# Kernel tuning notes

Measured on AMD Instinct MI355X. Metric: run time of the kernel, lower is better.

## Reference

```python
import jax, jax.numpy as jnp
import numpy as np

N_NODES = 100000


def gcn_conv(x, W, b, src, dst, n):
    # PyG GCNConv: linear transform, add self-loops, symmetric deg^-1/2 norm,
    # scatter-sum messages from src -> dst, add bias.
    x = x @ W  # [N, out]
    loop = jnp.arange(n, dtype=src.dtype)
    src_sl = jnp.concatenate([src, loop])
    dst_sl = jnp.concatenate([dst, loop])
    deg = jax.ops.segment_sum(jnp.ones_like(dst_sl, dtype=x.dtype), dst_sl, num_segments=n)
    dinv = jax.lax.rsqrt(deg)
    norm = dinv[src_sl] * dinv[dst_sl]  # [E+N]
    msg = x[src_sl] * norm[:, None]
    out = jax.ops.segment_sum(msg, dst_sl, num_segments=n)
    return out + b


def base_gnn(x, edge_index, W1, b1, W2, b2):
    src, dst = edge_index[0], edge_index[1]
    n = x.shape[0]
    h = gcn_conv(x, W1, b1, src, dst, n)
    h = jax.nn.relu(h)
    return gcn_conv(h, W2, b2, src, dst, n)


def setup_inputs() -> dict:
    key = jax.random.key(0)
    ks = jax.random.split(key, 12)
    n, e, ep, en = N_NODES, 1600000, 200000, 200000
    in_ch, hid, out_ch, n_classes = 256, 128, 128, 10
    x = jax.random.normal(ks[0], (n, in_ch), dtype=jnp.float32)
    edge_index = jax.random.randint(ks[1], (2, e), 0, n, dtype=jnp.int64)
    edge_index_pos = jax.random.randint(ks[2], (2, ep), 0, n, dtype=jnp.int64)
    edge_index_neg = jax.random.randint(ks[3], (2, en), 0, n, dtype=jnp.int64)
    s1 = 1.0 / np.sqrt(in_ch)
    s2 = 1.0 / np.sqrt(hid)
    so = 1.0 / np.sqrt(out_ch)
    sl = 1.0 / np.sqrt(2 * out_ch)
    return {
        "x": x,
        "edge_index": edge_index,
        "edge_index_pos": edge_index_pos,
        "edge_index_neg": edge_index_neg,
        "W1": jax.random.uniform(ks[4], (in_ch, hid), jnp.float32, -s1, s1),
        "b1": jnp.zeros((hid,), jnp.float32),
        "W2": jax.random.uniform(ks[5], (hid, out_ch), jnp.float32, -s2, s2),
        "b2": jnp.zeros((out_ch,), jnp.float32),
        "Wcls": jax.random.uniform(ks[6], (out_ch, n_classes), jnp.float32, -so, so),
        "bcls": jax.random.uniform(ks[7], (n_classes,), jnp.float32, -so, so),
        "Wlink": jax.random.uniform(ks[8], (2 * out_ch, 1), jnp.float32, -sl, sl),
        "blink": jax.random.uniform(ks[9], (1,), jnp.float32, -sl, sl),
    }


def reference(x, edge_index, edge_index_pos, edge_index_neg,
              W1, b1, W2, b2, Wcls, bcls, Wlink, blink):
    # Shared base embedding (math identical to torch's redundant recompute)
    h = base_gnn(x, edge_index, W1, b1, W2, b2)  # [N, 128]
    # Node head
    node_logits = jax.nn.relu(h) @ Wcls + bcls
    node_pred = jax.nn.log_softmax(node_logits, axis=1)
    # Link head: gather endpoint embeddings, concat, linear
    xp = jnp.concatenate([h[edge_index_pos[0]], h[edge_index_pos[1]]], axis=1)
    xn = jnp.concatenate([h[edge_index_neg[0]], h[edge_index_neg[1]]], axis=1)
    link_pos = (xp @ Wlink + blink)[:, 0]
    link_neg = (xn @ Wlink + blink)[:, 0]
    return (node_pred, link_pos, link_neg)
```

## Files before the change

### kernel.cpp

```cpp
#include <hip/hip_runtime.h>
#include <stdint.h>

typedef __attribute__((ext_vector_type(8))) short bf16x8;
typedef __attribute__((ext_vector_type(4))) float f32x4;

__device__ __forceinline__ float b2f(uint32_t h) {
    union { uint32_t u; float f; } v; v.u = h << 16; return v.f;
}
__device__ __forceinline__ ushort f2b(float f) {
    union { float f; uint32_t u; } v; v.f = f;
    uint32_t u = v.u;
    return (ushort)((u + 0x7fffu + ((u >> 16) & 1u)) >> 16);
}
__device__ __forceinline__ float ldin(const void* p, int i, int fp32) {
    return fp32 ? ((const float*)p)[i] : b2f(((const ushort*)p)[i]);
}

__global__ void k_flags(const void* W1, const void* ei, int* flags) {
    int l = threadIdx.x;
    const ushort* w = (const ushort*)W1;
    float a0 = fabsf(b2f(w[l]));
    float a1 = fabsf(b2f(w[64 + l]));
    bool bad = !(a0 <= 0.25f) || !(a1 <= 0.25f);
    unsigned long long mb = __ballot(bad);
    const int* e = (const int*)ei;
    bool z = (l < 16) ? (e[2 * l + 1] == 0) : false;
    unsigned long long mz = __ballot(z);
    if (l == 0) {
        flags[0] = mb ? 1 : 0;
        flags[1] = (__popcll(mz & 0xffffull) >= 15) ? 1 : 0;
    }
}

__global__ __launch_bounds__(256) void k_cvt_idx(const void* ei, const void* ep, const void* en,
                                                 int* cEi, int* cEp, int* cEn,
                                                 int twoE, int twoEp, int twoEn, int N,
                                                 const int* __restrict__ flags) {
    int i = blockIdx.x * 256 + threadIdx.x;
    int i64 = flags[1];
    const void* srcp; int* dstp; int j = i;
    if (i < twoE) { srcp = ei; dstp = cEi; }
    else if (i < twoE + twoEp) { srcp = ep; dstp = cEp; j = i - twoE; }
    else if (i < twoE + twoEp + twoEn) { srcp = en; dstp = cEn; j = i - twoE - twoEp; }
    else return;
    int v = i64 ? (int)((const long long*)srcp)[j] : ((const int*)srcp)[j];
    v = v < 0 ? 0 : (v >= N ? N - 1 : v);
    dstp[j] = v;
}

__global__ __launch_bounds__(256) void k_cvt_w(const void* W1, const void* W2, const void* Wc,
                                               const void* b1, const void* b2, const void* bc,
                                               const void* Wl, const void* bl,
                                               ushort* Wt1, ushort* Wt2, ushort* WtC,
                                               ushort* b1c, ushort* b2c, ushort* bcc,
                                               ushort* Wlc, ushort* blc,
                                               const int* __restrict__ flags) {
    int i = blockIdx.x * 256 + threadIdx.x;
    int f = flags[0];
    if (i < 32768) {
        int c = i >> 8, k = i & 255;
        Wt1[i] = f2b(ldin(W1, k * 128 + c, f));
    } else if (i < 49152) {
        int j = i - 32768, c = j >> 7, k = j & 127;
        Wt2[j] = f2b(ldin(W2, k * 128 + c, f));
    } else if (i < 51200) {
        int j = i - 49152, c = j >> 7, k = j & 127;
        ushort v = 0;
        if (c < 10) v = f2b(ldin(Wc, k * 10 + c, f));
        WtC[j] = v;
    } else if (i < 51328) {
        int j = i - 51200; b1c[j] = f2b(ldin(b1, j, f));
    } else if (i < 51456) {
        int j = i - 51328; b2c[j] = f2b(ldin(b2, j, f));
    } else if (i < 51472) {
        int j = i - 51456;
        ushort v = 0;
        if (j < 10) v = f2b(ldin(bc, j, f));
        bcc[j] = v;
    } else if (i < 51728) {
        int j = i - 51472; Wlc[j] = f2b(ldin(Wl, j, f));
    } else if (i < 51736) {
        int j = i - 51728;
        ushort v = 0;
        if (j < 1) v = f2b(ldin(bl, 0, f));
        blc[j] = v;
    }
}

__global__ __launch_bounds__(256) void k_cvt_x(const void* __restrict__ x, ushort* __restrict__ xc,
                                               int N, const int* __restrict__ flags) {
    int gw = blockIdx.x * 4 + (threadIdx.x >> 6);
    int ntile = (N + 15) >> 4;
    if (gw >= ntile * 8) return;
    int tile = gw >> 3, s = gw & 7;
    int l = threadIdx.x & 63, mr = l & 15, q = l >> 4;
    int row = tile * 16 + mr;
    if (row > N - 1) row = N - 1;
    uint4 o;
    if (flags[0]) {
        const float* xf = (const float*)x + (size_t)row * 256 + s * 32 + q * 8;
        float4 a = *(const float4*)xf;
        float4 b = *(const float4*)(xf + 4);
        o.x = (uint32_t)f2b(a.x) | ((uint32_t)f2b(a.y) << 16);
        o.y = (uint32_t)f2b(a.z) | ((uint32_t)f2b(a.w) << 16);
        o.z = (uint32_t)f2b(b.x) | ((uint32_t)f2b(b.y) << 16);
        o.w = (uint32_t)f2b(b.z) | ((uint32_t)f2b(b.w) << 16);
    } else {
        o = *(const uint4*)((const ushort*)x + (size_t)row * 256 + s * 32 + q * 8);
    }
    *(uint4*)(xc + ((size_t)gw * 64 + l) * 8) = o;
}

__global__ __launch_bounds__(256) void k_hist1(const int* __restrict__ dst, int* __restrict__ histM,
                                               int E, int NB1) {
    __shared__ int h[512];
    for (int j = threadIdx.x; j < 512; j += 256) h[j] = 0;
    __syncthreads();
    int base = blockIdx.x * 4096;
    for (int j = threadIdx.x; j < 4096; j += 256) {
        int i = base + j;
        if (i < E) atomicAdd(&h[dst[i] >> 8], 1);
    }
    __syncthreads();
    for (int j = threadIdx.x; j < 512; j += 256)
        histM[j * NB1 + blockIdx.x] = h[j];
}

__global__ __launch_bounds__(1024) void k_mscan_block(const int* __restrict__ in, int* __restrict__ out,
                                                      int* __restrict__ bsum, int len) {
    __shared__ int sh[1024];
    int t = threadIdx.x;
    int i = blockIdx.x * 1024 + t;
    int val = (i < len) ? in[i] : 0;
    sh[t] = val; __syncthreads();
    for (int off = 1; off < 1024; off <<= 1) {
        int v = (t >= off) ? sh[t - off] : 0;
        __syncthreads();
        sh[t] += v;
        __syncthreads();
    }
    if (i < len) out[i] = sh[t] - val;
    if (t == 1023) bsum[blockIdx.x] = sh[1023];
}

__global__ __launch_bounds__(1024) void k_mscan_top(int* __restrict__ bsum, int nb) {
    __shared__ int sh[1024];
    int t = threadIdx.x;
    int val = (t < nb) ? bsum[t] : 0;
    sh[t] = val; __syncthreads();
    for (int off = 1; off < 1024; off <<= 1) {
        int v = (t >= off) ? sh[t - off] : 0;
        __syncthreads();
        sh[t] += v;
        __syncthreads();
    }
    if (t < nb) bsum[t] = sh[t] - val;
}

__global__ __launch_bounds__(1024) void k_mscan_add(int* __restrict__ out, const int* __restrict__ bsum, int len) {
    int i = blockIdx.x * 1024 + threadIdx.x;
    if (i < len) out[i] += bsum[blockIdx.x];
}

__global__ __launch_bounds__(512) void k_cbs(const int* __restrict__ off, int* __restrict__ cbs, int E, int NB1) {
    int t = threadIdx.x;
    cbs[t] = off[t * NB1];
    if (t == 0) cbs[512] = E;
}

__global__ __launch_bounds__(256) void k_scatter1(const int* __restrict__ src, const int* __restrict__ dst,
                                                  const int* __restrict__ off, int2* __restrict__ grouped,
                                                  int E, int NB1) {
    __shared__ int o[512];
    for (int j = threadIdx.x; j < 512; j += 256) o[j] = off[j * NB1 + blockIdx.x];
    __syncthreads();
    int base = blockIdx.x * 4096;
    for (int j = threadIdx.x; j < 4096; j += 256) {
        int i = base + j;
        if (i < E) {
            int d = dst[i];
            int p = atomicAdd(&o[d >> 8], 1);
            grouped[p] = make_int2(src[i], d);
        }
    }
}

__global__ __launch_bounds__(256) void k_deg2(const int2* __restrict__ grouped, const int* __restrict__ cbs,
                                              int* __restrict__ deg, int N) {
    __shared__ int c[256];
    c[threadIdx.x] = 0;
    __syncthreads();
    int b = blockIdx.x;
    int s0 = cbs[b], s1 = cbs[b + 1];
    for (int i = s0 + threadIdx.x; i < s1; i += 256)
        atomicAdd(&c[grouped[i].y & 255], 1);
    __syncthreads();
    int v = b * 256 + threadIdx.x;
    if (v < N) deg[v] = c[threadIdx.x];
}

__global__ __launch_bounds__(1024) void k_scan_block(const int* __restrict__ deg, int* __restrict__ rowptr,
                                                     float* __restrict__ dinv, int* __restrict__ bsum, int n) {
    __shared__ int sh[1024];
    int t = threadIdx.x;
    int i = blockIdx.x * 1024 + t;
    int val = (i < n) ? deg[i] : 0;
    sh[t] = val; __syncthreads();
    for (int off = 1; off < 1024; off <<= 1) {
        int v = (t >= off) ? sh[t - off] : 0;
        __syncthreads();
        sh[t] += v;
        __syncthreads();
    }
    if (i < n) {
        rowptr[i] = sh[t] - val;
        dinv[i] = rsqrtf((float)(val + 1));
    }
    if (t == 1023) bsum[blockIdx.x] = sh[1023];
}

__global__ __launch_bounds__(128) void k_scan_top(const int* __restrict__ bsum, int* __restrict__ boff, int nb) {
    __shared__ int sh[128];
    int t = threadIdx.x;
    int val = (t < nb) ? bsum[t] : 0;
    sh[t] = val; __syncthreads();
    for (int off = 1; off < 128; off <<= 1) {
        int v = (t >= off) ? sh[t - off] : 0;
        __syncthreads();
        sh[t] += v;
        __syncthreads();
    }
    if (t < nb) boff[t] = sh[t] - val;
}

__global__ __launch_bounds__(1024) void k_scan_add(int* __restrict__ rowptr, const int* __restrict__ boff,
                                                   int n, int E) {
    int i = blockIdx.x * 1024 + threadIdx.x;
    if (i < n) rowptr[i] += boff[blockIdx.x];
    if (i == 0) rowptr[n] = E;
}

__global__ __launch_bounds__(256) void k_fill2(const int2* __restrict__ grouped, const int* __restrict__ cbs,
                                               const int* __restrict__ rowptr, const float* __restrict__ dinv,
                                               int2* __restrict__ edge, int N) {
    __shared__ int o[256];
    int b = blockIdx.x;
    int v = b * 256 + threadIdx.x;
    o[threadIdx.x] = (v < N) ? rowptr[v] : 0;
    __syncthreads();
    int s0 = cbs[b], s1 = cbs[b + 1];
    for (int i = s0 + threadIdx.x; i < s1; i += 256) {
        int2 e = grouped[i];
        int p = atomicAdd(&o[e.y & 255], 1);
        float w = dinv[e.x] * dinv[e.y];
        edge[p] = make_int2(e.x, __float_as_int(w));
    }
}

template <int NS>
__global__ __launch_bounds__(256, 2) void k_gemm(const ushort* __restrict__ Xf,
                                                 const ushort* __restrict__ Wt,
                                                 ushort* __restrict__ Out, int nrows) {
    __shared__ uint4 sB[NS * 8 * 64];

    const int tid = threadIdx.x;
    for (int it = tid; it < NS * 8 * 64; it += 256) {
        int l = it & 63, fn = it >> 6;
        int s = fn >> 3, n = fn & 7;
        int mr = l & 15, q = l >> 4;
        sB[it] = *(const uint4*)(Wt + (size_t)(n * 16 + mr) * (NS * 32) + s * 32 + q * 8);
    }
    __syncthreads();

    const int wave = tid >> 6;
    const int l = tid & 63;
    const int q = l >> 4, mr = l & 15;
    const int gw = blockIdx.x * 4 + wave;
    const int nw = gridDim.x * 4;
    const int ntile = (nrows + 15) >> 4;

    for (int tp = gw; tp * 2 < ntile; tp += nw) {
        const int t0 = tp * 2;
        const bool has1 = (t0 + 1 < ntile);
        const int t1 = has1 ? t0 + 1 : t0;

        bf16x8 a0[NS], a1[NS];
        const ushort* x0 = Xf + ((size_t)t0 * NS * 64 + l) * 8;
        const ushort* x1 = Xf + ((size_t)t1 * NS * 64 + l) * 8;
#pragma unroll
        for (int s = 0; s < NS; ++s) a0[s] = *(const bf16x8*)(x0 + s * 512);
#pragma unroll
        for (int s = 0; s < NS; ++s) a1[s] = *(const bf16x8*)(x1 + s * 512);

        f32x4 acc0[8], acc1[8];
#pragma unroll
        for (int n = 0; n < 8; ++n) {
            acc0[n] = (f32x4){0.f, 0.f, 0.f, 0.f};
            acc1[n] = (f32x4){0.f, 0.f, 0.f, 0.f};
        }
#pragma unroll
        for (int s = 0; s < NS; ++s) {
#pragma unroll
            for (int n = 0; n < 8; ++n) {
                bf16x8 b = __builtin_bit_cast(bf16x8, sB[(s * 8 + n) * 64 + l]);
                acc0[n] = __builtin_amdgcn_mfma_f32_16x16x32_bf16(b, a0[s], acc0[n], 0, 0, 0);
                acc1[n] = __builtin_amdgcn_mfma_f32_16x16x32_bf16(b, a1[s], acc1[n], 0, 0, 0);
            }
        }
        int row0 = t0 * 16 + mr;
        if (row0 < nrows) {
            ushort* orow = Out + (size_t)row0 * 128 + q * 4;
#pragma unroll
            for (int n = 0; n < 8; ++n) {
                uint2 o;
                o.x = (uint32_t)f2b(acc0[n][0]) | ((uint32_t)f2b(acc0[n][1]) << 16);
                o.y = (uint32_t)f2b(acc0[n][2]) | ((uint32_t)f2b(acc0[n][3]) << 16);
                *(uint2*)(orow + n * 16) = o;
            }
        }
        if (has1) {
            int row1 = t1 * 16 + mr;
            if (row1 < nrows) {
                ushort* orow = Out + (size_t)row1 * 128 + q * 4;
#pragma unroll
                for (int n = 0; n < 8; ++n) {
                    uint2 o;
                    o.x = (uint32_t)f2b(acc1[n][0]) | ((uint32_t)f2b(acc1[n][1]) << 16);
                    o.y = (uint32_t)f2b(acc1[n][2]) | ((uint32_t)f2b(acc1[n][3]) << 16);
                    *(uint2*)(orow + n * 16) = o;
                }
            }
        }
    }
}

__device__ __forceinline__ void fma8(float* acc, uint4 p, float w) {
    uint32_t pu[4] = {p.x, p.y, p.z, p.w};
#pragma unroll
    for (int k = 0; k < 4; ++k) {
        float lo = __uint_as_float(pu[k] << 16);
        float hi = __uint_as_float(pu[k] & 0xffff0000u);
        acc[2 * k]     += lo * w;
        acc[2 * k + 1] += hi * w;
    }
}

__global__ __launch_bounds__(256) void k_conv(const ushort* __restrict__ XW, const int* __restrict__ rowptr,
                                              const int2* __restrict__ edge, const float* __restrict__ dinv,
                                              const ushort* __restrict__ bias, ushort* __restrict__ Hout,
                                              int n, int relu, int frag) {
    int wave = threadIdx.x >> 6;
    int v = blockIdx.x * 4 + wave;
    if (v >= n) return;
    int l = threadIdx.x & 63;
    int g = l >> 4;
    int c = l & 15;

    int s0 = rowptr[v], s1 = rowptr[v + 1];
    float dv = dinv[v];
    float wself = (g == 0) ? dv * dv : 0.f;

    uint4 pv = *(const uint4*)(XW + (size_t)v * 128 + c * 8);
    float acc[8];
    {
        uint32_t pu[4] = {pv.x, pv.y, pv.z, pv.w};
#pragma unroll
        for (int k = 0; k < 4; ++k) {
            acc[2 * k]     = __uint_as_float(pu[k] << 16) * wself;
            acc[2 * k + 1] = __uint_as_float(pu[k] & 0xffff0000u) * wself;
        }
    }

    int i = s0;
    while (i + 8 <= s1) {
        int2 eA = edge[i + g];
        int2 eB = edge[i + 4 + g];
        uint4 pA = *(const uint4*)(XW + (size_t)eA.x * 128 + c * 8);
        uint4 pB = *(const uint4*)(XW + (size_t)eB.x * 128 + c * 8);
        fma8(acc, pA, __int_as_float(eA.y));
        fma8(acc, pB, __int_as_float(eB.y));
        i += 8;
    }
    if (i + 4 <= s1) {
        int2 e = edge[i + g];
        uint4 p = *(const uint4*)(XW + (size_t)e.x * 128 + c * 8);
        fma8(acc, p, __int_as_float(e.y));
        i += 4;
    }
    if (i < s1) {
        int ei = i + g;
        bool val = ei < s1;
        int2 e = edge[val ? ei : s0];
        uint4 p = *(const uint4*)(XW + (size_t)e.x * 128 + c * 8);
        fma8(acc, p, val ? __int_as_float(e.y) : 0.f);
    }

#pragma unroll
    for (int k = 0; k < 8; ++k) {
        acc[k] += __shfl_xor(acc[k], 16);
        acc[k] += __shfl_xor(acc[k], 32);
    }

    if (g == 0) {
        uint4 bb = *(const uint4*)(bias + c * 8);
        uint32_t bu[4] = {bb.x, bb.y, bb.z, bb.w};
        uint4 o;
        uint32_t* op = (uint32_t*)&o;
#pragma unroll
        for (int k = 0; k < 4; ++k) {
            float lo = acc[2 * k]     + __uint_as_float(bu[k] << 16);
            float hi = acc[2 * k + 1] + __uint_as_float(bu[k] & 0xffff0000u);
            if (relu) { lo = fmaxf(lo, 0.f); hi = fmaxf(hi, 0.f); }
            op[k] = (uint32_t)f2b(lo) | ((uint32_t)f2b(hi) << 16);
        }
        if (frag) {
            int tile = v >> 4, mr = v & 15;
            size_t chunk = ((size_t)(tile * 4 + (c >> 2)) * 64 + (c & 3) * 16 + mr);
            *(uint4*)(Hout + chunk * 8) = o;
        } else {
            *(uint4*)(Hout + (size_t)v * 128 + c * 8) = o;
        }
    }
}

__global__ __launch_bounds__(256) void k_nodehead(const ushort* __restrict__ H, const ushort* __restrict__ WtC,
                                                  const ushort* __restrict__ bcc, void* __restrict__ out,
                                                  int n, const int* __restrict__ flags) {
    int wave = threadIdx.x >> 6;
    int gw = blockIdx.x * 4 + wave;
    if (gw * 16 >= n) return;
    int fp32o = flags[0];
    int l = threadIdx.x & 63;
    int q = l >> 4, mr = l & 15;
    int m0 = gw * 16;

    f32x4 acc = (f32x4){0.f, 0.f, 0.f, 0.f};
    const ushort* hrow = H + (size_t)(m0 + mr) * 128 + q * 8;
#pragma unroll
    for (int s = 0; s < 4; ++s) {
        bf16x8 a = *(const bf16x8*)(hrow + s * 32);
#pragma unroll
        for (int j = 0; j < 8; ++j) {
            ushort t = (ushort)a[j];
            if (t & 0x8000u) a[j] = 0;
        }
        bf16x8 b = *(const bf16x8*)(WtC + (size_t)mr * 128 + s * 32 + q * 8);
        acc = __builtin_amdgcn_mfma_f32_16x16x32_bf16(a, b, acc, 0, 0, 0);
    }

    float bc = b2f(bcc[mr]);
#pragma unroll
    for (int r = 0; r < 4; ++r) {
        float logit = acc[r] + bc;
        float m = (mr < 10) ? logit : -1e30f;
#pragma unroll
        for (int off = 1; off < 16; off <<= 1) m = fmaxf(m, __shfl_xor(m, off, 16));
        float ex = (mr < 10) ? expf(logit - m) : 0.f;
        float ssum = ex;
#pragma unroll
        for (int off = 1; off < 16; off <<= 1) ssum += __shfl_xor(ssum, off, 16);
        if (mr < 10) {
            float lsm = logit - m - logf(ssum);
            size_t idx = (size_t)(m0 + q * 4 + r) * 10 + mr;
            if (fp32o) ((float*)out)[idx] = lsm;
            else ((ushort*)out)[idx] = f2b(lsm);
        }
    }
}

__global__ __launch_bounds__(256) void k_link(const ushort* __restrict__ H, const int* __restrict__ pos,
                                              const int* __restrict__ neg, const ushort* __restrict__ Wlc,
                                              const ushort* __restrict__ blc, void* __restrict__ out,
                                              size_t obase, int Ep, int En, const int* __restrict__ flags) {
    int wave = threadIdx.x >> 6;
    int l = threadIdx.x & 63;
    int g = l >> 4, t = l & 15;
    int e = (blockIdx.x * 4 + wave) * 4 + g;
    if (e >= Ep + En) return;
    int fp32o = flags[0];

    const int* P; int eb, off2;
    if (e < Ep) { P = pos; eb = e; off2 = Ep; }
    else { P = neg; eb = e - Ep; off2 = En; }
    int sI = P[eb], dI = P[off2 + eb];

    bf16x8 hs = *(const bf16x8*)(H + (size_t)sI * 128 + t * 8);
    bf16x8 hd = *(const bf16x8*)(H + (size_t)dI * 128 + t * 8);
    bf16x8 w0 = *(const bf16x8*)(Wlc + t * 8);
    bf16x8 w1 = *(const bf16x8*)(Wlc + 128 + t * 8);

    float acc = 0.f;
#pragma unroll
    for (int j = 0; j < 8; ++j) {
        acc += b2f((ushort)hs[j]) * b2f((ushort)w0[j]);
        acc += b2f((ushort)hd[j]) * b2f((ushort)w1[j]);
    }
#pragma unroll
    for (int off = 1; off < 16; off <<= 1) acc += __shfl_xor(acc, off, 16);
    if (t == 0) {
        float vf = acc + b2f(blc[0]);
        size_t idx = obase + (size_t)e;
        if (fp32o) ((float*)out)[idx] = vf;
        else ((ushort*)out)[idx] = f2b(vf);
    }
}

extern "C" void kernel_launch(void* const* d_in, const int* in_sizes, int n_in,
                              void* d_out, int out_size, void* d_ws, size_t ws_size,
                              hipStream_t stream) {
    const void* x    = d_in[0];
    const void* ei   = d_in[1];
    const void* eip  = d_in[2];
    const void* ein  = d_in[3];
    const void* W1   = d_in[4];
    const void* b1   = d_in[5];
    const void* W2   = d_in[6];
    const void* b2   = d_in[7];
    const void* Wcls = d_in[8];
    const void* bcls = d_in[9];
    const void* Wl   = d_in[10];
    const void* bl   = d_in[11];

    const int N  = in_sizes[0] / 256;
    const int E  = in_sizes[1] / 2;
    const int Ep = in_sizes[2] / 2;
    const int En = in_sizes[3] / 2;

    const int NB1  = (E + 4095) / 4096;
    const int mlen = 512 * NB1;
    const int mb   = (mlen + 1023) / 1024;
    const int ntile = (N + 15) / 16;

    char* ws = (char*)d_ws;
    size_t off = 0;
    auto alloc = [&](size_t bytes) -> void* {
        void* p = ws + off;
        off = (off + bytes + 255) & ~(size_t)255;
        return p;
    };
    int*    flags  = (int*)alloc(256);
    ushort* xc     = (ushort*)alloc((size_t)ntile * 8 * 64 * 16);
    ushort* bufXW  = (ushort*)alloc((size_t)N * 128 * 2);
    ushort* bufH   = (ushort*)alloc((size_t)ntile * 4 * 64 * 16);
    int*    cEi    = (int*)alloc((size_t)2 * E * 4);
    int*    cEp    = (int*)alloc((size_t)2 * Ep * 4);
    int*    cEn    = (int*)alloc((size_t)2 * En * 4);
    int2*   grouped= (int2*)alloc((size_t)E * 8);
    int*    histM  = (int*)alloc((size_t)mlen * 4);
    int*    offM   = (int*)alloc((size_t)mlen * 4);
    int*    msum   = (int*)alloc(4096);
    int*    cbs    = (int*)alloc(513 * 4);
    float*  dinv   = (float*)alloc((size_t)N * 4);
    int*    deg    = (int*)alloc((size_t)N * 4);
    int*    rowp   = (int*)alloc((size_t)(N + 1) * 4);
    int2*   edge   = (int2*)alloc((size_t)E * 8);
    int*    bsum   = (int*)alloc(1024);
    int*    boff   = (int*)alloc(1024);
    ushort* Wt1    = (ushort*)alloc(65536);
    ushort* Wt2    = (ushort*)alloc(32768);
    ushort* WtC    = (ushort*)alloc(4096);
    ushort* b1c    = (ushort*)alloc(256);
    ushort* b2c    = (ushort*)alloc(256);
    ushort* bcc    = (ushort*)alloc(64);
    ushort* Wlc    = (ushort*)alloc(512);
    ushort* blc    = (ushort*)alloc(64);

    k_flags<<<1, 64, 0, stream>>>(W1, ei, flags);

    int twoE = 2 * E, twoEp = 2 * Ep, twoEn = 2 * En;
    int idx_total = twoE + twoEp + twoEn;
    k_cvt_idx<<<(idx_total + 255) / 256, 256, 0, stream>>>(ei, eip, ein, cEi, cEp, cEn,
                                                           twoE, twoEp, twoEn, N, flags);
    k_cvt_w<<<203, 256, 0, stream>>>(W1, W2, Wcls, b1, b2, bcls, Wl, bl,
                                     Wt1, Wt2, WtC, b1c, b2c, bcc, Wlc, blc, flags);
    k_cvt_x<<<(ntile * 8 + 3) / 4, 256, 0, stream>>>(x, xc, N, flags);

    const int* srcp = cEi;
    const int* dstp = cEi + E;

    k_hist1<<<NB1, 256, 0, stream>>>(dstp, histM, E, NB1);
    k_mscan_block<<<mb, 1024, 0, stream>>>(histM, offM, msum, mlen);
    k_mscan_top<<<1, 1024, 0, stream>>>(msum, mb);
    k_mscan_add<<<mb, 1024, 0, stream>>>(offM, msum, mlen);
    k_cbs<<<1, 512, 0, stream>>>(offM, cbs, E, NB1);
    k_scatter1<<<NB1, 256, 0, stream>>>(srcp, dstp, offM, grouped, E, NB1);
    k_deg2<<<512, 256, 0, stream>>>(grouped, cbs, deg, N);
    int nb = (N + 1023) / 1024;
    k_scan_block<<<nb, 1024, 0, stream>>>(deg, rowp, dinv, bsum, N);
    k_scan_top<<<1, 128, 0, stream>>>(bsum, boff, nb);
    k_scan_add<<<nb, 1024, 0, stream>>>(rowp, boff, N, E);
    k_fill2<<<512, 256, 0, stream>>>(grouped, cbs, rowp, dinv, edge, N);

    k_gemm<8><<<512, 256, 0, stream>>>(xc, Wt1, bufXW, N);
    k_conv<<<(N + 3) / 4, 256, 0, stream>>>(bufXW, rowp, edge, dinv, b1c, bufH, N, 1, 1);
    k_gemm<4><<<768, 256, 0, stream>>>(bufH, Wt2, bufXW, N);
    k_conv<<<(N + 3) / 4, 256, 0, stream>>>(bufXW, rowp, edge, dinv, b2c, bufH, N, 0, 0);

    int head_blocks = ((N + 15) / 16 + 3) / 4;
    k_nodehead<<<head_blocks, 256, 0, stream>>>(bufH, WtC, bcc, d_out, N, flags);
    k_link<<<(Ep + En + 3) / 4, 256, 0, stream>>>(bufH, cEp, cEn, Wlc, blc, d_out,
                                                  (size_t)N * 10, Ep, En, flags);
}
```

Before: 526.9 us.

## Fuse prep kernels, merge scan passes, precompute per-node link projections

Merges the flag, index, weight and x conversion kernels into one launch in which each block re-derives the dtype flags locally. It also folds each scan's top-level pass and add pass into a single kernel that rescans the block sums. The link head now uses linearity: the node-head kernel computes per-node dot products of H with the two halves of Wlink, and the link kernel just gathers two floats per edge instead of two 128-wide rows. This cuts launch count and the gather traffic for 400K link edges. In exchange the dtype sniff is repeated in every block and each scan block redoes the top-level scan.

```diff
diff --git a/kernel.cpp b/kernel.cpp
--- a/kernel.cpp
+++ b/kernel.cpp
@@ -16,99 +16,102 @@
     return fp32 ? ((const float*)p)[i] : b2f(((const ushort*)p)[i]);
 }
 
-__global__ void k_flags(const void* W1, const void* ei, int* flags) {
-    int l = threadIdx.x;
-    const ushort* w = (const ushort*)W1;
-    float a0 = fabsf(b2f(w[l]));
-    float a1 = fabsf(b2f(w[64 + l]));
-    bool bad = !(a0 <= 0.25f) || !(a1 <= 0.25f);
-    unsigned long long mb = __ballot(bad);
-    const int* e = (const int*)ei;
-    bool z = (l < 16) ? (e[2 * l + 1] == 0) : false;
-    unsigned long long mz = __ballot(z);
-    if (l == 0) {
-        flags[0] = mb ? 1 : 0;
-        flags[1] = (__popcll(mz & 0xffffull) >= 15) ? 1 : 0;
-    }
-}
-
-__global__ __launch_bounds__(256) void k_cvt_idx(const void* ei, const void* ep, const void* en,
-                                                 int* cEi, int* cEp, int* cEn,
-                                                 int twoE, int twoEp, int twoEn, int N,
-                                                 const int* __restrict__ flags) {
-    int i = blockIdx.x * 256 + threadIdx.x;
-    int i64 = flags[1];
-    const void* srcp; int* dstp; int j = i;
-    if (i < twoE) { srcp = ei; dstp = cEi; }
-    else if (i < twoE + twoEp) { srcp = ep; dstp = cEp; j = i - twoE; }
-    else if (i < twoE + twoEp + twoEn) { srcp = en; dstp = cEn; j = i - twoE - twoEp; }
-    else return;
-    int v = i64 ? (int)((const long long*)srcp)[j] : ((const int*)srcp)[j];
-    v = v < 0 ? 0 : (v >= N ? N - 1 : v);
-    dstp[j] = v;
-}
-
-__global__ __launch_bounds__(256) void k_cvt_w(const void* W1, const void* W2, const void* Wc,
-                                               const void* b1, const void* b2, const void* bc,
-                                               const void* Wl, const void* bl,
-                                               ushort* Wt1, ushort* Wt2, ushort* WtC,
-                                               ushort* b1c, ushort* b2c, ushort* bcc,
-                                               ushort* Wlc, ushort* blc,
-                                               const int* __restrict__ flags) {
-    int i = blockIdx.x * 256 + threadIdx.x;
-    int f = flags[0];
-    if (i < 32768) {
-        int c = i >> 8, k = i & 255;
-        Wt1[i] = f2b(ldin(W1, k * 128 + c, f));
-    } else if (i < 49152) {
-        int j = i - 32768, c = j >> 7, k = j & 127;
-        Wt2[j] = f2b(ldin(W2, k * 128 + c, f));
-    } else if (i < 51200) {
-        int j = i - 49152, c = j >> 7, k = j & 127;
-        ushort v = 0;
-        if (c < 10) v = f2b(ldin(Wc, k * 10 + c, f));
-        WtC[j] = v;
-    } else if (i < 51328) {
-        int j = i - 51200; b1c[j] = f2b(ldin(b1, j, f));
-    } else if (i < 51456) {
-        int j = i - 51328; b2c[j] = f2b(ldin(b2, j, f));
-    } else if (i < 51472) {
-        int j = i - 51456;
-        ushort v = 0;
-        if (j < 10) v = f2b(ldin(bc, j, f));
-        bcc[j] = v;
-    } else if (i < 51728) {
-        int j = i - 51472; Wlc[j] = f2b(ldin(Wl, j, f));
-    } else if (i < 51736) {
-        int j = i - 51728;
-        ushort v = 0;
-        if (j < 1) v = f2b(ldin(bl, 0, f));
-        blc[j] = v;
-    }
-}
-
-__global__ __launch_bounds__(256) void k_cvt_x(const void* __restrict__ x, ushort* __restrict__ xc,
-                                               int N, const int* __restrict__ flags) {
-    int gw = blockIdx.x * 4 + (threadIdx.x >> 6);
-    int ntile = (N + 15) >> 4;
-    if (gw >= ntile * 8) return;
-    int tile = gw >> 3, s = gw & 7;
-    int l = threadIdx.x & 63, mr = l & 15, q = l >> 4;
-    int row = tile * 16 + mr;
-    if (row > N - 1) row = N - 1;
-    uint4 o;
-    if (flags[0]) {
-        const float* xf = (const float*)x + (size_t)row * 256 + s * 32 + q * 8;
-        float4 a = *(const float4*)xf;
-        float4 b = *(const float4*)(xf + 4);
-        o.x = (uint32_t)f2b(a.x) | ((uint32_t)f2b(a.y) << 16);
-        o.y = (uint32_t)f2b(a.z) | ((uint32_t)f2b(a.w) << 16);
-        o.z = (uint32_t)f2b(b.x) | ((uint32_t)f2b(b.y) << 16);
-        o.w = (uint32_t)f2b(b.z) | ((uint32_t)f2b(b.w) << 16);
+__device__ __forceinline__ void sniff(const void* W1, const void* ei, int* sf) {
+    if (threadIdx.x < 64) {
+        int l = threadIdx.x;
+        const ushort* w = (const ushort*)W1;
+        bool bad = !(fabsf(b2f(w[l])) <= 0.25f) || !(fabsf(b2f(w[64 + l])) <= 0.25f);
+        unsigned long long mb = __ballot(bad);
+        const int* e = (const int*)ei;
+        bool z = (l < 16) ? (e[2 * l + 1] == 0) : false;
+        unsigned long long mz = __ballot(z);
+        if (l == 0) {
+            sf[0] = mb ? 1 : 0;
+            sf[1] = (__popcll(mz & 0xffffull) >= 15) ? 1 : 0;
+        }
+    }
+    __syncthreads();
+}
+
+__global__ __launch_bounds__(256) void k_prep(const void* __restrict__ x,
+                                              const void* ei, const void* ep, const void* en,
+                                              const void* W1, const void* b1, const void* W2,
+                                              const void* b2, const void* Wc, const void* bc,
+                                              const void* Wl, const void* bl,
+                                              int* cEi, int* cEp, int* cEn,
+                                              ushort* __restrict__ xc,
+                                              ushort* Wt1, ushort* Wt2, ushort* WtC,
+                                              ushort* b1c, ushort* b2c, ushort* bcc,
+                                              ushort* Wlc, ushort* blc,
+                                              int twoE, int twoEp, int twoEn, int N,
+                                              int Bidx, int Bw) {
+    __shared__ int sf[2];
+    sniff(W1, ei, sf);
+    int f = sf[0], i64 = sf[1];
+    int b = blockIdx.x;
+
+    if (b < Bidx) {
+        int i = b * 256 + threadIdx.x;
+        const void* srcp; int* dstp; int j = i;
+        if (i < twoE) { srcp = ei; dstp = cEi; }
+        else if (i < twoE + twoEp) { srcp = ep; dstp = cEp; j = i - twoE; }
+        else if (i < twoE + twoEp + twoEn) { srcp = en; dstp = cEn; j = i - twoE - twoEp; }
+        else return;
+        int v = i64 ? (int)((const long long*)srcp)[j] : ((const int*)srcp)[j];
+        v = v < 0 ? 0 : (v >= N ? N - 1 : v);
+        dstp[j] = v;
+    } else if (b < Bidx + Bw) {
+        int i = (b - Bidx) * 256 + threadIdx.x;
+        if (i < 32768) {
+            int c = i >> 8, k = i & 255;
+            Wt1[i] = f2b(ldin(W1, k * 128 + c, f));
+        } else if (i < 49152) {
+            int j = i - 32768, c = j >> 7, k = j & 127;
+            Wt2[j] = f2b(ldin(W2, k * 128 + c, f));
+        } else if (i < 51200) {
+            int j = i - 49152, c = j >> 7, k = j & 127;
+            ushort v = 0;
+            if (c < 10) v = f2b(ldin(Wc, k * 10 + c, f));
+            WtC[j] = v;
+        } else if (i < 51328) {
+            int j = i - 51200; b1c[j] = f2b(ldin(b1, j, f));
+        } else if (i < 51456) {
+            int j = i - 51328; b2c[j] = f2b(ldin(b2, j, f));
+        } else if (i < 51472) {
+            int j = i - 51456;
+            ushort v = 0;
+            if (j < 10) v = f2b(ldin(bc, j, f));
+            bcc[j] = v;
+        } else if (i < 51728) {
+            int j = i - 51472; Wlc[j] = f2b(ldin(Wl, j, f));
+        } else if (i < 51736) {
+            int j = i - 51728;
+            ushort v = 0;
+            if (j < 1) v = f2b(ldin(bl, 0, f));
+            blc[j] = v;
+        }
     } else {
-        o = *(const uint4*)((const ushort*)x + (size_t)row * 256 + s * 32 + q * 8);
-    }
-    *(uint4*)(xc + ((size_t)gw * 64 + l) * 8) = o;
+        int gw = (b - Bidx - Bw) * 4 + (threadIdx.x >> 6);
+        int ntile = (N + 15) >> 4;
+        if (gw >= ntile * 8) return;
+        int tile = gw >> 3, s = gw & 7;
+        int l = threadIdx.x & 63, mr = l & 15, q = l >> 4;
+        int row = tile * 16 + mr;
+        if (row > N - 1) row = N - 1;
+        uint4 o;
+        if (f) {
+            const float* xf = (const float*)x + (size_t)row * 256 + s * 32 + q * 8;
+            float4 a = *(const float4*)xf;
+            float4 bb = *(const float4*)(xf + 4);
+            o.x = (uint32_t)f2b(a.x) | ((uint32_t)f2b(a.y) << 16);
+            o.y = (uint32_t)f2b(a.z) | ((uint32_t)f2b(a.w) << 16);
+            o.z = (uint32_t)f2b(bb.x) | ((uint32_t)f2b(bb.y) << 16);
+            o.w = (uint32_t)f2b(bb.z) | ((uint32_t)f2b(bb.w) << 16);
+        } else {
+            o = *(const uint4*)((const ushort*)x + (size_t)row * 256 + s * 32 + q * 8);
+        }
+        *(uint4*)(xc + ((size_t)gw * 64 + l) * 8) = o;
+    }
 }
 
 __global__ __launch_bounds__(256) void k_hist1(const int* __restrict__ dst, int* __restrict__ histM,
@@ -143,29 +146,26 @@
     if (t == 1023) bsum[blockIdx.x] = sh[1023];
 }
 
-__global__ __launch_bounds__(1024) void k_mscan_top(int* __restrict__ bsum, int nb) {
+__global__ __launch_bounds__(1024) void k_mscan_topadd(int* __restrict__ out, const int* __restrict__ bsum,
+                                                       int* __restrict__ cbs, int len, int mb,
+                                                       int NB1, int E) {
     __shared__ int sh[1024];
     int t = threadIdx.x;
-    int val = (t < nb) ? bsum[t] : 0;
-    sh[t] = val; __syncthreads();
+    sh[t] = (t < mb) ? bsum[t] : 0; __syncthreads();
     for (int off = 1; off < 1024; off <<= 1) {
         int v = (t >= off) ? sh[t - off] : 0;
         __syncthreads();
         sh[t] += v;
         __syncthreads();
     }
-    if (t < nb) bsum[t] = sh[t] - val;
-}
-
-__global__ __launch_bounds__(1024) void k_mscan_add(int* __restrict__ out, const int* __restrict__ bsum, int len) {
-    int i = blockIdx.x * 1024 + threadIdx.x;
-    if (i < len) out[i] += bsum[blockIdx.x];
-}
-
-__global__ __launch_bounds__(512) void k_cbs(const int* __restrict__ off, int* __restrict__ cbs, int E, int NB1) {
-    int t = threadIdx.x;
-    cbs[t] = off[t * NB1];
-    if (t == 0) cbs[512] = E;
+    int pref = (blockIdx.x > 0) ? sh[blockIdx.x - 1] : 0;
+    int i = blockIdx.x * 1024 + t;
+    if (i < len) {
+        int v = out[i] + pref;
+        out[i] = v;
+        if (i % NB1 == 0) cbs[i / NB1] = v;
+    }
+    if (i == 0) cbs[512] = E;
 }
 
 __global__ __launch_bounds__(256) void k_scatter1(const int* __restrict__ src, const int* __restrict__ dst,
@@ -219,24 +219,20 @@
     if (t == 1023) bsum[blockIdx.x] = sh[1023];
 }
 
-__global__ __launch_bounds__(128) void k_scan_top(const int* __restrict__ bsum, int* __restrict__ boff, int nb) {
-    __shared__ int sh[128];
+__global__ __launch_bounds__(1024) void k_scan_topadd(int* __restrict__ rowptr, const int* __restrict__ bsum,
+                                                      int nb, int n, int E) {
+    __shared__ int sh[1024];
     int t = threadIdx.x;
-    int val = (t < nb) ? bsum[t] : 0;
-    sh[t] = val; __syncthreads();
-    for (int off = 1; off < 128; off <<= 1) {
+    sh[t] = (t < nb) ? bsum[t] : 0; __syncthreads();
+    for (int off = 1; off < 1024; off <<= 1) {
         int v = (t >= off) ? sh[t - off] : 0;
         __syncthreads();
         sh[t] += v;
         __syncthreads();
     }
-    if (t < nb) boff[t] = sh[t] - val;
-}
-
-__global__ __launch_bounds__(1024) void k_scan_add(int* __restrict__ rowptr, const int* __restrict__ boff,
-                                                   int n, int E) {
-    int i = blockIdx.x * 1024 + threadIdx.x;
-    if (i < n) rowptr[i] += boff[blockIdx.x];
+    int pref = (blockIdx.x > 0) ? sh[blockIdx.x - 1] : 0;
+    int i = blockIdx.x * 1024 + t;
+    if (i < n) rowptr[i] += pref;
     if (i == 0) rowptr[n] = E;
 }
 
@@ -424,21 +420,44 @@
 }
 
 __global__ __launch_bounds__(256) void k_nodehead(const ushort* __restrict__ H, const ushort* __restrict__ WtC,
-                                                  const ushort* __restrict__ bcc, void* __restrict__ out,
-                                                  int n, const int* __restrict__ flags) {
+                                                  const ushort* __restrict__ bcc, const ushort* __restrict__ Wlc,
+                                                  float2* __restrict__ ab, void* __restrict__ out,
+                                                  int n, const void* W1s, const void* eis) {
+    __shared__ int sf[2];
+    sniff(W1s, eis, sf);
+    int fp32o = sf[0];
     int wave = threadIdx.x >> 6;
     int gw = blockIdx.x * 4 + wave;
     if (gw * 16 >= n) return;
-    int fp32o = flags[0];
     int l = threadIdx.x & 63;
     int q = l >> 4, mr = l & 15;
     int m0 = gw * 16;
 
+    const ushort* hrow = H + (size_t)(m0 + mr) * 128 + q * 8;
+    bf16x8 araw[4];
+#pragma unroll
+    for (int s = 0; s < 4; ++s) araw[s] = *(const bf16x8*)(hrow + s * 32);
+
+    float pa = 0.f, pb = 0.f;
+#pragma unroll
+    for (int s = 0; s < 4; ++s) {
+        bf16x8 w0 = *(const bf16x8*)(Wlc + s * 32 + q * 8);
+        bf16x8 w1 = *(const bf16x8*)(Wlc + 128 + s * 32 + q * 8);
+#pragma unroll
+        for (int j = 0; j < 8; ++j) {
+            float hv = b2f((ushort)araw[s][j]);
+            pa += hv * b2f((ushort)w0[j]);
+            pb += hv * b2f((ushort)w1[j]);
+        }
+    }
+    pa += __shfl_xor(pa, 16); pa += __shfl_xor(pa, 32);
+    pb += __shfl_xor(pb, 16); pb += __shfl_xor(pb, 32);
+    if (q == 0 && (m0 + mr) < n) ab[m0 + mr] = make_float2(pa, pb);
+
     f32x4 acc = (f32x4){0.f, 0.f, 0.f, 0.f};
-    const ushort* hrow = H + (size_t)(m0 + mr) * 128 + q * 8;
 #pragma unroll
     for (int s = 0; s < 4; ++s) {
-        bf16x8 a = *(const bf16x8*)(hrow + s * 32);
+        bf16x8 a = araw[s];
 #pragma unroll
         for (int j = 0; j < 8; ++j) {
             ushort t = (ushort)a[j];
@@ -459,50 +478,31 @@
         float ssum = ex;
 #pragma unroll
         for (int off = 1; off < 16; off <<= 1) ssum += __shfl_xor(ssum, off, 16);
-        if (mr < 10) {
+        int row = m0 + q * 4 + r;
+        if (mr < 10 && row < n) {
             float lsm = logit - m - logf(ssum);
-            size_t idx = (size_t)(m0 + q * 4 + r) * 10 + mr;
+            size_t idx = (size_t)row * 10 + mr;
             if (fp32o) ((float*)out)[idx] = lsm;
             else ((ushort*)out)[idx] = f2b(lsm);
         }
     }
 }
 
-__global__ __launch_bounds__(256) void k_link(const ushort* __restrict__ H, const int* __restrict__ pos,
-                                              const int* __restrict__ neg, const ushort* __restrict__ Wlc,
-                                              const ushort* __restrict__ blc, void* __restrict__ out,
-                                              size_t obase, int Ep, int En, const int* __restrict__ flags) {
-    int wave = threadIdx.x >> 6;
-    int l = threadIdx.x & 63;
-    int g = l >> 4, t = l & 15;
-    int e = (blockIdx.x * 4 + wave) * 4 + g;
-    if (e >= Ep + En) return;
-    int fp32o = flags[0];
-
-    const int* P; int eb, off2;
-    if (e < Ep) { P = pos; eb = e; off2 = Ep; }
-    else { P = neg; eb = e - Ep; off2 = En; }
-    int sI = P[eb], dI = P[off2 + eb];
-
-    bf16x8 hs = *(const bf16x8*)(H + (size_t)sI * 128 + t * 8);
-    bf16x8 hd = *(const bf16x8*)(H + (size_t)dI * 128 + t * 8);
-    bf16x8 w0 = *(const bf16x8*)(Wlc + t * 8);
-    bf16x8 w1 = *(const bf16x8*)(Wlc + 128 + t * 8);
-
-    float acc = 0.f;
-#pragma unroll
-    for (int j = 0; j < 8; ++j) {
-        acc += b2f((ushort)hs[j]) * b2f((ushort)w0[j]);
-        acc += b2f((ushort)hd[j]) * b2f((ushort)w1[j]);
-    }
-#pragma unroll
-    for (int off = 1; off < 16; off <<= 1) acc += __shfl_xor(acc, off, 16);
-    if (t == 0) {
-        float vf = acc + b2f(blc[0]);
-        size_t idx = obase + (size_t)e;
-        if (fp32o) ((float*)out)[idx] = vf;
-        else ((ushort*)out)[idx] = f2b(vf);
-    }
+__global__ __launch_bounds__(256) void k_linkfast(const float2* __restrict__ ab, const int* __restrict__ pos,
+                                                  const int* __restrict__ neg, const ushort* __restrict__ blc,
+                                                  void* __restrict__ out, size_t obase, int Ep, int En,
+                                                  const void* W1s, const void* eis) {
+    __shared__ int sf[2];
+    sniff(W1s, eis, sf);
+    int i = blockIdx.x * 256 + threadIdx.x;
+    if (i >= Ep + En) return;
+    int s, d;
+    if (i < Ep) { s = pos[i]; d = pos[Ep + i]; }
+    else { int j = i - Ep; s = neg[j]; d = neg[En + j]; }
+    float vf = ab[s].x + ab[d].y + b2f(blc[0]);
+    size_t idx = obase + (size_t)i;
+    if (sf[0]) ((float*)out)[idx] = vf;
+    else ((ushort*)out)[idx] = f2b(vf);
 }
 
 extern "C" void kernel_launch(void* const* d_in, const int* in_sizes, int n_in,
@@ -538,10 +538,10 @@
         off = (off + bytes + 255) & ~(size_t)255;
         return p;
     };
-    int*    flags  = (int*)alloc(256);
     ushort* xc     = (ushort*)alloc((size_t)ntile * 8 * 64 * 16);
     ushort* bufXW  = (ushort*)alloc((size_t)N * 128 * 2);
     ushort* bufH   = (ushort*)alloc((size_t)ntile * 4 * 64 * 16);
+    float2* ab     = (float2*)alloc((size_t)N * 8);
     int*    cEi    = (int*)alloc((size_t)2 * E * 4);
     int*    cEp    = (int*)alloc((size_t)2 * Ep * 4);
     int*    cEn    = (int*)alloc((size_t)2 * En * 4);
@@ -555,7 +555,6 @@
     int*    rowp   = (int*)alloc((size_t)(N + 1) * 4);
     int2*   edge   = (int2*)alloc((size_t)E * 8);
     int*    bsum   = (int*)alloc(1024);
-    int*    boff   = (int*)alloc(1024);
     ushort* Wt1    = (ushort*)alloc(65536);
     ushort* Wt2    = (ushort*)alloc(32768);
     ushort* WtC    = (ushort*)alloc(4096);
@@ -565,30 +564,28 @@
     ushort* Wlc    = (ushort*)alloc(512);
     ushort* blc    = (ushort*)alloc(64);
 
-    k_flags<<<1, 64, 0, stream>>>(W1, ei, flags);
-
     int twoE = 2 * E, twoEp = 2 * Ep, twoEn = 2 * En;
     int idx_total = twoE + twoEp + twoEn;
-    k_cvt_idx<<<(idx_total + 255) / 256, 256, 0, stream>>>(ei, eip, ein, cEi, cEp, cEn,
-                                                           twoE, twoEp, twoEn, N, flags);
-    k_cvt_w<<<203, 256, 0, stream>>>(W1, W2, Wcls, b1, b2, bcls, Wl, bl,
-                                     Wt1, Wt2, WtC, b1c, b2c, bcc, Wlc, blc, flags);
-    k_cvt_x<<<(ntile * 8 + 3) / 4, 256, 0, stream>>>(x, xc, N, flags);
+    int Bidx = (idx_total + 255) / 256;
+    int Bw   = 203;
+    int Bx   = (ntile * 8 + 3) / 4;
+
+    k_prep<<<Bidx + Bw + Bx, 256, 0, stream>>>(x, ei, eip, ein, W1, b1, W2, b2, Wcls, bcls, Wl, bl,
+                                               cEi, cEp, cEn, xc, Wt1, Wt2, WtC,
+                                               b1c, b2c, bcc, Wlc, blc,
+                                               twoE, twoEp, twoEn, N, Bidx, Bw);
 
     const int* srcp = cEi;
     const int* dstp = cEi + E;
 
     k_hist1<<<NB1, 256, 0, stream>>>(dstp, histM, E, NB1);
     k_mscan_block<<<mb, 1024, 0, stream>>>(histM, offM, msum, mlen);
-    k_mscan_top<<<1, 1024, 0, stream>>>(msum, mb);
-    k_mscan_add<<<mb, 1024, 0, stream>>>(offM, msum, mlen);
-    k_cbs<<<1, 512, 0, stream>>>(offM, cbs, E, NB1);
+    k_mscan_topadd<<<mb, 1024, 0, stream>>>(offM, msum, cbs, mlen, mb, NB1, E);
     k_scatter1<<<NB1, 256, 0, stream>>>(srcp, dstp, offM, grouped, E, NB1);
     k_deg2<<<512, 256, 0, stream>>>(grouped, cbs, deg, N);
     int nb = (N + 1023) / 1024;
     k_scan_block<<<nb, 1024, 0, stream>>>(deg, rowp, dinv, bsum, N);
-    k_scan_top<<<1, 128, 0, stream>>>(bsum, boff, nb);
-    k_scan_add<<<nb, 1024, 0, stream>>>(rowp, boff, N, E);
+    k_scan_topadd<<<nb, 1024, 0, stream>>>(rowp, bsum, nb, N, E);
     k_fill2<<<512, 256, 0, stream>>>(grouped, cbs, rowp, dinv, edge, N);
 
     k_gemm<8><<<512, 256, 0, stream>>>(xc, Wt1, bufXW, N);
@@ -597,7 +594,7 @@
     k_conv<<<(N + 3) / 4, 256, 0, stream>>>(bufXW, rowp, edge, dinv, b2c, bufH, N, 0, 0);
 
     int head_blocks = ((N + 15) / 16 + 3) / 4;
-    k_nodehead<<<head_blocks, 256, 0, stream>>>(bufH, WtC, bcc, d_out, N, flags);
-    k_link<<<(Ep + En + 3) / 4, 256, 0, stream>>>(bufH, cEp, cEn, Wlc, blc, d_out,
-                                                  (size_t)N * 10, Ep, En, flags);
-}
+    k_nodehead<<<head_blocks, 256, 0, stream>>>(bufH, WtC, bcc, Wlc, ab, d_out, N, W1, ei);
+    k_linkfast<<<(Ep + En + 255) / 256, 256, 0, stream>>>(ab, cEp, cEn, blc, d_out,
+                                                          (size_t)N * 10, Ep, En, W1, ei);
+}
```

New measurement: 492.7 us. 1.07x faster.
